# Optimization experiments

Measured on AMD Instinct MI355X. Metric: run time of the kernel, lower is better.

Reference implementation:

```python
import jax, jax.numpy as jnp
import numpy as np

DECAY = 0.99
EPSILON = 1e-05
CODEBOOK_SIZE = 1024


def setup_inputs() -> dict:
    key = jax.random.key(0)
    k1, k2, k3 = jax.random.split(key, 3)
    B, T, D, K = 8, 4096, 128, CODEBOOK_SIZE
    return {
        "x": jax.random.normal(k1, (B, T, D), dtype=jnp.float32),
        "embed": jax.random.normal(k2, (K, D), dtype=jnp.float32),
        "cluster_size": jnp.ones((K,), dtype=jnp.float32),
        "embed_avg": jax.random.normal(k3, (K, D), dtype=jnp.float32),
    }


def reference(x, embed, cluster_size, embed_avg):
    shape = x.shape
    K, D = embed.shape
    flat = x.reshape(-1, D)  # (N, D)

    dist = 2.0 * (flat @ embed.T) - jnp.sum(flat * flat, axis=1, keepdims=True) \
           - jnp.sum(embed * embed, axis=1)[None, :]  # (N, K)
    embed_ind_flat = jnp.argmax(dist, axis=-1)  # (N,) int
    embed_ind = embed_ind_flat.reshape(shape[:-1])
    quantize = embed[embed_ind]  # dequantize via gather, (B, T, D)

    # training EMA updates (one-hot scatter expressed as segment sums)
    counts = jax.ops.segment_sum(jnp.ones_like(embed_ind_flat, dtype=x.dtype),
                                 embed_ind_flat, num_segments=K)  # == onehot.sum(0)
    embed_sum = jax.ops.segment_sum(flat, embed_ind_flat, num_segments=K)  # == (x.T @ onehot).T

    new_cluster_size = cluster_size * DECAY + (1.0 - DECAY) * counts
    new_embed_avg = embed_avg * DECAY + (1.0 - DECAY) * embed_sum

    total = new_cluster_size.sum()
    smoothed = (new_cluster_size + EPSILON) / (total + K * EPSILON) * total
    new_embed = new_embed_avg / smoothed[:, None]

    return quantize, embed_ind, new_cluster_size, new_embed_avg, new_embed
```

## Files before the change

kernel.cpp:

```cpp
#include <hip/hip_runtime.h>

#define NROWS 32768
#define DDIM  128
#define KCODES 1024
#define DECAY 0.99f
#define OMD   0.01f
#define EPS   1e-5f

typedef __attribute__((ext_vector_type(8))) short short8;
typedef __attribute__((ext_vector_type(4))) float f32x4;

#define WS_COUNTS 0
#define WS_OFFS   1024
#define WS_CURSOR 2048
#define WS_INV    3072
#define WS_EN2H   4096
#define WS_BUCKET 5120

__device__ __forceinline__ unsigned int f2bf(float f) {
  union { float f; unsigned int u; } cv; cv.f = f;
  unsigned int u = cv.u;
  return (u + 0x7fffu + ((u >> 16) & 1u)) >> 16;
}

__global__ __launch_bounds__(256) void pack_e(const float* __restrict__ embed,
                                              ushort* __restrict__ epack,
                                              float* __restrict__ en2h,
                                              int* __restrict__ cnt0) {
  const int tid = threadIdx.x;
  if (blockIdx.x == 0) {
    #pragma unroll
    for (int i = 0; i < 4; ++i) cnt0[tid + i * 256] = 0;
  }
  const int w = tid >> 6, lane = tid & 63;
  const int nt = blockIdx.x * 4 + w;
  const int m = lane & 15, q = lane >> 4;
  const int row = nt * 16 + m;
  const float* ep = embed + (size_t)row * DDIM + q * 8;
  float ss = 0.f;
  #pragma unroll
  for (int kb = 0; kb < 4; ++kb) {
    float4 v0 = *(const float4*)(ep + kb * 32);
    float4 v1 = *(const float4*)(ep + kb * 32 + 4);
    float v[8] = {v0.x, v0.y, v0.z, v0.w, v1.x, v1.y, v1.z, v1.w};
    unsigned int h[8], l[8];
    #pragma unroll
    for (int j = 0; j < 8; ++j) {
      ss += v[j] * v[j];
      h[j] = f2bf(v[j]);
      float fh = __uint_as_float(h[j] << 16);
      l[j] = f2bf(v[j] - fh);
    }
    uint4 ph, pl;
    ph.x = h[0] | (h[1] << 16); ph.y = h[2] | (h[3] << 16);
    ph.z = h[4] | (h[5] << 16); ph.w = h[6] | (h[7] << 16);
    pl.x = l[0] | (l[1] << 16); pl.y = l[2] | (l[3] << 16);
    pl.z = l[4] | (l[5] << 16); pl.w = l[6] | (l[7] << 16);
    *(uint4*)(epack + (((size_t)nt * 8 + kb) * 64 + lane) * 8)     = ph;
    *(uint4*)(epack + (((size_t)nt * 8 + kb + 4) * 64 + lane) * 8) = pl;
  }
  ss += __shfl_xor(ss, 16, 64);
  ss += __shfl_xor(ss, 32, 64);
  if (q == 0) en2h[row] = 0.5f * ss;
}

__global__ __launch_bounds__(256) void vq_mfma(
    const float* __restrict__ x, const short8* __restrict__ ep8,
    const float* __restrict__ en2h, const float* __restrict__ embed,
    float* __restrict__ out_ind, float* __restrict__ out_q,
    int* __restrict__ cnt_i) {
  __shared__ unsigned long long keys[4][32];
  __shared__ int scodes[32];
  const int tid = threadIdx.x;
  const int w = tid >> 6, lane = tid & 63;
  const int c = lane & 15, q = lane >> 4;
  const int mt0 = blockIdx.x * 2;

  short8 a[2][8];
  #pragma unroll
  for (int t = 0; t < 2; ++t) {
    const float* xp = x + (size_t)((mt0 + t) * 16 + c) * DDIM + q * 8;
    #pragma unroll
    for (int kb = 0; kb < 4; ++kb) {
      float4 v0 = *(const float4*)(xp + kb * 32);
      float4 v1 = *(const float4*)(xp + kb * 32 + 4);
      float v[8] = {v0.x, v0.y, v0.z, v0.w, v1.x, v1.y, v1.z, v1.w};
      short8 hh, ll;
      #pragma unroll
      for (int j = 0; j < 8; ++j) {
        unsigned int hv = f2bf(v[j]);
        hh[j] = (short)hv;
        float fh = __uint_as_float(hv << 16);
        ll[j] = (short)f2bf(v[j] - fh);
      }
      a[t][kb] = hh;
      a[t][kb + 4] = ll;
    }
  }

  float bestv[8]; int besti[8];
  #pragma unroll
  for (int i = 0; i < 8; ++i) { bestv[i] = -3.4e38f; besti[i] = 0; }

  const int nt0 = w * 16;
  const int ph = blockIdx.x & 15;

  auto stage = [&](short8 (&st)[8], float& nh, int i) {
    const int nt = nt0 + ((ph + i) & 15);
    const short8* p = ep8 + (size_t)nt * 512 + lane;
    #pragma unroll
    for (int j = 0; j < 8; ++j) st[j] = p[j * 64];
    nh = en2h[nt * 16 + c];
  };

  auto proc = [&](const short8 (&st)[8], float nh, int i) {
    const int nt = nt0 + ((ph + i) & 15);
    f32x4 acc0 = {-nh, -nh, -nh, -nh};
    f32x4 acc1 = acc0;
    __builtin_amdgcn_s_setprio(1);
    #pragma unroll
    for (int kb = 0; kb < 4; ++kb) {
      acc0 = __builtin_amdgcn_mfma_f32_16x16x32_bf16(a[0][kb], st[kb], acc0, 0, 0, 0);
      acc1 = __builtin_amdgcn_mfma_f32_16x16x32_bf16(a[1][kb], st[kb], acc1, 0, 0, 0);
    }
    #pragma unroll
    for (int kb = 0; kb < 4; ++kb) {
      acc0 = __builtin_amdgcn_mfma_f32_16x16x32_bf16(a[0][kb + 4], st[kb], acc0, 0, 0, 0);
      acc1 = __builtin_amdgcn_mfma_f32_16x16x32_bf16(a[1][kb + 4], st[kb], acc1, 0, 0, 0);
    }
    #pragma unroll
    for (int kb = 0; kb < 4; ++kb) {
      acc0 = __builtin_amdgcn_mfma_f32_16x16x32_bf16(a[0][kb], st[kb + 4], acc0, 0, 0, 0);
      acc1 = __builtin_amdgcn_mfma_f32_16x16x32_bf16(a[1][kb], st[kb + 4], acc1, 0, 0, 0);
    }
    __builtin_amdgcn_s_setprio(0);
    const int code = nt * 16 + c;
    #pragma unroll
    for (int r = 0; r < 4; ++r) {
      float v0 = acc0[r];
      if (v0 > bestv[r] || (v0 == bestv[r] && code < besti[r])) {
        bestv[r] = v0; besti[r] = code;
      }
      float v1 = acc1[r];
      if (v1 > bestv[4 + r] || (v1 == bestv[4 + r] && code < besti[4 + r])) {
        bestv[4 + r] = v1; besti[4 + r] = code;
      }
    }
  };

  short8 sA[8], sB[8];
  float nhA, nhB;
  stage(sA, nhA, 0);

  for (int i = 0; i < 14; i += 2) {
    stage(sB, nhB, i + 1);
    __builtin_amdgcn_sched_barrier(0);
    proc(sA, nhA, i);
    stage(sA, nhA, i + 2);
    __builtin_amdgcn_sched_barrier(0);
    proc(sB, nhB, i + 1);
  }
  stage(sB, nhB, 15);
  __builtin_amdgcn_sched_barrier(0);
  proc(sA, nhA, 14);
  proc(sB, nhB, 15);

  #pragma unroll
  for (int off = 1; off < 16; off <<= 1) {
    #pragma unroll
    for (int i = 0; i < 8; ++i) {
      float ov = __shfl_xor(bestv[i], off, 64);
      int   oi = __shfl_xor(besti[i], off, 64);
      if (ov > bestv[i] || (ov == bestv[i] && oi < besti[i])) {
        bestv[i] = ov; besti[i] = oi;
      }
    }
  }
  if (c == 0) {
    #pragma unroll
    for (int t = 0; t < 2; ++t)
      #pragma unroll
      for (int r = 0; r < 4; ++r) {
        unsigned u = __float_as_uint(bestv[t * 4 + r]);
        unsigned su = (u & 0x80000000u) ? ~u : (u | 0x80000000u);
        keys[w][t * 16 + q * 4 + r] =
            ((unsigned long long)su << 32) |
            (unsigned long long)(0xFFFFFFFFu - (unsigned)besti[t * 4 + r]);
      }
  }
  __syncthreads();
  if (tid < 32) {
    unsigned long long k0 = keys[0][tid], k1 = keys[1][tid];
    unsigned long long k2 = keys[2][tid], k3 = keys[3][tid];
    unsigned long long k = k0 > k1 ? k0 : k1;
    if (k2 > k) k = k2;
    if (k3 > k) k = k3;
    int code = (int)(0xFFFFFFFFu - (unsigned)(k & 0xFFFFFFFFull));
    out_ind[blockIdx.x * 32 + tid] = (float)code;
    scodes[tid] = code;
    atomicAdd(&cnt_i[code], 1);
  }
  __syncthreads();
  #pragma unroll
  for (int it = 0; it < 4; ++it) {
    int idx = tid + it * 256;
    int row = idx >> 5, c4 = idx & 31;
    int code = scodes[row];
    *(float4*)(out_q + (size_t)(blockIdx.x * 32 + row) * DDIM + c4 * 4) =
        *(const float4*)(embed + (size_t)code * DDIM + c4 * 4);
  }
}

__global__ __launch_bounds__(1024) void scan_fin(
    int* offs, const float* __restrict__ cs,
    float* __restrict__ counts_g, int* __restrict__ cursor,
    float* __restrict__ inv, float* __restrict__ out_ncs) {
  __shared__ float wtot[16], ctot[16];
  const int tid = threadIdx.x;
  const int lane = tid & 63, w = tid >> 6;
  const int cnt = offs[tid];
  const float cnum = (float)cnt;
  const float cv = cs[tid];
  float s = cnum;
  #pragma unroll
  for (int off = 1; off < 64; off <<= 1) {
    float v = __shfl_up(s, off, 64);
    if (lane >= off) s += v;
  }
  float r2 = cv;
  #pragma unroll
  for (int off = 32; off > 0; off >>= 1) r2 += __shfl_down(r2, off, 64);
  if (lane == 63) wtot[w] = s;
  if (lane == 0)  ctot[w] = r2;
  __syncthreads();
  if (tid < 16) {
    float v = wtot[tid];
    #pragma unroll
    for (int off = 1; off < 16; off <<= 1) {
      float p = __shfl_up(v, off, 64);
      if (tid >= off) v += p;
    }
    wtot[tid] = v;
    float t2 = ctot[tid];
    #pragma unroll
    for (int off = 8; off > 0; off >>= 1) t2 += __shfl_down(t2, off, 64);
    if (tid == 0) ctot[0] = t2;
  }
  __syncthreads();
  const float prefix = (w > 0) ? wtot[w - 1] : 0.f;
  const int excl = (int)(s + prefix) - cnt;
  offs[tid] = excl;
  cursor[tid] = excl;
  counts_g[tid] = cnum;
  const float ncs = cv * DECAY + OMD * cnum;
  out_ncs[tid] = ncs;
  const float total = ctot[0] * DECAY + OMD * (float)NROWS;
  inv[tid] = (total + (float)KCODES * EPS) / ((ncs + EPS) * total);
}

__global__ void scatter_rows(const float* __restrict__ out_ind,
                             int* __restrict__ cursor, int* __restrict__ bucket) {
  int row = blockIdx.x * 256 + threadIdx.x;
  int code = (int)out_ind[row];
  int pos = atomicAdd(cursor + code, 1);
  bucket[pos] = row;
}

__global__ __launch_bounds__(256) void esum_fin(
    const int* __restrict__ bucket, const int* __restrict__ offs,
    const float* __restrict__ counts, const float* __restrict__ x,
    const float* __restrict__ ea, const float* __restrict__ inv,
    float* __restrict__ out_nea, float* __restrict__ out_ne) {
  __shared__ float4 part[512];
  const int code = blockIdx.x;
  const int t = threadIdx.x;
  const int c8 = t & 15;
  const int h = t >> 4;
  const int start = offs[code];
  const int cnt = (int)counts[code];
  float4 a0 = {0.f, 0.f, 0.f, 0.f}, a1 = {0.f, 0.f, 0.f, 0.f};
  int i = h;
  for (; i + 16 < cnt; i += 32) {
    int rowA = bucket[start + i];
    int rowB = bucket[start + i + 16];
    const float* pa = x + (size_t)rowA * DDIM + c8 * 8;
    const float* pb = x + (size_t)rowB * DDIM + c8 * 8;
    float4 xa0 = *(const float4*)(pa), xa1 = *(const float4*)(pa + 4);
    float4 xb0 = *(const float4*)(pb), xb1 = *(const float4*)(pb + 4);
    a0.x += xa0.x + xb0.x; a0.y += xa0.y + xb0.y; a0.z += xa0.z + xb0.z; a0.w += xa0.w + xb0.w;
    a1.x += xa1.x + xb1.x; a1.y += xa1.y + xb1.y; a1.z += xa1.z + xb1.z; a1.w += xa1.w + xb1.w;
  }
  for (; i < cnt; i += 16) {
    int row = bucket[start + i];
    const float* pa = x + (size_t)row * DDIM + c8 * 8;
    float4 xa0 = *(const float4*)(pa), xa1 = *(const float4*)(pa + 4);
    a0.x += xa0.x; a0.y += xa0.y; a0.z += xa0.z; a0.w += xa0.w;
    a1.x += xa1.x; a1.y += xa1.y; a1.z += xa1.z; a1.w += xa1.w;
  }
  part[h * 32 + c8 * 2]     = a0;
  part[h * 32 + c8 * 2 + 1] = a1;
  __syncthreads();
  if (t < 32) {
    float4 s = part[t];
    #pragma unroll
    for (int hh = 1; hh < 16; ++hh) {
      float4 p = part[hh * 32 + t];
      s.x += p.x; s.y += p.y; s.z += p.z; s.w += p.w;
    }
    float iv = inv[code];
    int base = code * DDIM + t * 4;
    float4 a = *(const float4*)(ea + base);
    float4 nea;
    nea.x = a.x * DECAY + OMD * s.x; nea.y = a.y * DECAY + OMD * s.y;
    nea.z = a.z * DECAY + OMD * s.z; nea.w = a.w * DECAY + OMD * s.w;
    *(float4*)(out_nea + base) = nea;
    float4 ne;
    ne.x = nea.x * iv; ne.y = nea.y * iv; ne.z = nea.z * iv; ne.w = nea.w * iv;
    *(float4*)(out_ne + base) = ne;
  }
}

extern "C" void kernel_launch(void* const* d_in, const int* in_sizes, int n_in,
                              void* d_out, int out_size, void* d_ws, size_t ws_size,
                              hipStream_t stream) {
  const float* x     = (const float*)d_in[0];
  const float* embed = (const float*)d_in[1];
  const float* cs    = (const float*)d_in[2];
  const float* ea    = (const float*)d_in[3];

  float* out     = (float*)d_out;
  float* out_q   = out;
  float* out_ind = out_q + 4194304;
  float* out_ncs = out_ind + 32768;
  float* out_nea = out_ncs + 1024;
  float* out_ne  = out_nea + 131072;

  float* ws     = (float*)d_ws;
  float* counts = ws + WS_COUNTS;
  int*   offs   = (int*)(ws + WS_OFFS);
  int*   cursor = (int*)(ws + WS_CURSOR);
  float* inv    = ws + WS_INV;
  float* en2h   = ws + WS_EN2H;
  int*   bucket = (int*)(ws + WS_BUCKET);

  ushort* epack = (ushort*)out_nea;

  pack_e<<<16, 256, 0, stream>>>(embed, epack, en2h, offs);
  vq_mfma<<<NROWS / 32, 256, 0, stream>>>(x, (const short8*)epack, en2h, embed,
                                          out_ind, out_q, offs);
  scan_fin<<<1, 1024, 0, stream>>>(offs, cs, counts, cursor, inv, out_ncs);
  scatter_rows<<<NROWS / 256, 256, 0, stream>>>(out_ind, cursor, bucket);
  esum_fin<<<KCODES, 256, 0, stream>>>(bucket, offs, counts, x, ea, inv,
                                       out_nea, out_ne);
}
```

Measured before the change: 166.1 us.

## Replace global bucket sort with per-code scan of indices in esum kernel

```diff
diff --git a/kernel.cpp b/kernel.cpp
--- a/kernel.cpp
+++ b/kernel.cpp
@@ -10,12 +10,8 @@
 typedef __attribute__((ext_vector_type(8))) short short8;
 typedef __attribute__((ext_vector_type(4))) float f32x4;
 
-#define WS_COUNTS 0
-#define WS_OFFS   1024
-#define WS_CURSOR 2048
-#define WS_INV    3072
-#define WS_EN2H   4096
-#define WS_BUCKET 5120
+#define WS_CSSUM 0
+#define WS_EN2H  1024
 
 __device__ __forceinline__ unsigned int f2bf(float f) {
   union { float f; unsigned int u; } cv; cv.f = f;
@@ -26,12 +22,10 @@
 __global__ __launch_bounds__(256) void pack_e(const float* __restrict__ embed,
                                               ushort* __restrict__ epack,
                                               float* __restrict__ en2h,
-                                              int* __restrict__ cnt0) {
+                                              const float* __restrict__ cs,
+                                              float* __restrict__ cssum) {
+  __shared__ float ws4[4];
   const int tid = threadIdx.x;
-  if (blockIdx.x == 0) {
-    #pragma unroll
-    for (int i = 0; i < 4; ++i) cnt0[tid + i * 256] = 0;
-  }
   const int w = tid >> 6, lane = tid & 63;
   const int nt = blockIdx.x * 4 + w;
   const int m = lane & 15, q = lane >> 4;
@@ -62,13 +56,21 @@
   ss += __shfl_xor(ss, 16, 64);
   ss += __shfl_xor(ss, 32, 64);
   if (q == 0) en2h[row] = 0.5f * ss;
+
+  if (blockIdx.x == 0) {
+    float s = cs[tid] + cs[tid + 256] + cs[tid + 512] + cs[tid + 768];
+    #pragma unroll
+    for (int off = 1; off < 64; off <<= 1) s += __shfl_xor(s, off, 64);
+    if (lane == 0) ws4[w] = s;
+    __syncthreads();
+    if (tid == 0) cssum[0] = ws4[0] + ws4[1] + ws4[2] + ws4[3];
+  }
 }
 
 __global__ __launch_bounds__(256) void vq_mfma(
     const float* __restrict__ x, const short8* __restrict__ ep8,
     const float* __restrict__ en2h, const float* __restrict__ embed,
-    float* __restrict__ out_ind, float* __restrict__ out_q,
-    int* __restrict__ cnt_i) {
+    float* __restrict__ out_ind, float* __restrict__ out_q) {
   __shared__ unsigned long long keys[4][32];
   __shared__ int scodes[32];
   const int tid = threadIdx.x;
@@ -103,18 +105,15 @@
   for (int i = 0; i < 8; ++i) { bestv[i] = -3.4e38f; besti[i] = 0; }
 
   const int nt0 = w * 16;
-  const int ph = blockIdx.x & 15;
 
   auto stage = [&](short8 (&st)[8], float& nh, int i) {
-    const int nt = nt0 + ((ph + i) & 15);
-    const short8* p = ep8 + (size_t)nt * 512 + lane;
+    const short8* p = ep8 + (size_t)(nt0 + i) * 512 + lane;
     #pragma unroll
     for (int j = 0; j < 8; ++j) st[j] = p[j * 64];
-    nh = en2h[nt * 16 + c];
+    nh = en2h[(nt0 + i) * 16 + c];
   };
 
   auto proc = [&](const short8 (&st)[8], float nh, int i) {
-    const int nt = nt0 + ((ph + i) & 15);
     f32x4 acc0 = {-nh, -nh, -nh, -nh};
     f32x4 acc1 = acc0;
     __builtin_amdgcn_s_setprio(1);
@@ -134,36 +133,31 @@
       acc1 = __builtin_amdgcn_mfma_f32_16x16x32_bf16(a[1][kb], st[kb + 4], acc1, 0, 0, 0);
     }
     __builtin_amdgcn_s_setprio(0);
-    const int code = nt * 16 + c;
+    const int code = (nt0 + i) * 16 + c;
     #pragma unroll
     for (int r = 0; r < 4; ++r) {
-      float v0 = acc0[r];
-      if (v0 > bestv[r] || (v0 == bestv[r] && code < besti[r])) {
-        bestv[r] = v0; besti[r] = code;
-      }
-      float v1 = acc1[r];
-      if (v1 > bestv[4 + r] || (v1 == bestv[4 + r] && code < besti[4 + r])) {
-        bestv[4 + r] = v1; besti[4 + r] = code;
-      }
+      if (acc0[r] > bestv[r])     { bestv[r] = acc0[r];     besti[r] = code; }
+      if (acc1[r] > bestv[4 + r]) { bestv[4 + r] = acc1[r]; besti[4 + r] = code; }
     }
   };
 
-  short8 sA[8], sB[8];
-  float nhA, nhB;
+  short8 sA[8], sB[8], sC[8];
+  float nhA, nhB, nhC;
   stage(sA, nhA, 0);
-
-  for (int i = 0; i < 14; i += 2) {
-    stage(sB, nhB, i + 1);
+  stage(sB, nhB, 1);
+
+  for (int t = 0; t < 15; t += 3) {
+    stage(sC, nhC, t + 2);
     __builtin_amdgcn_sched_barrier(0);
-    proc(sA, nhA, i);
-    stage(sA, nhA, i + 2);
+    proc(sA, nhA, t);
+    stage(sA, nhA, (t + 3 > 15) ? 15 : t + 3);
     __builtin_amdgcn_sched_barrier(0);
-    proc(sB, nhB, i + 1);
-  }
-  stage(sB, nhB, 15);
-  __builtin_amdgcn_sched_barrier(0);
-  proc(sA, nhA, 14);
-  proc(sB, nhB, 15);
+    proc(sB, nhB, t + 1);
+    stage(sB, nhB, (t + 4 > 15) ? 15 : t + 4);
+    __builtin_amdgcn_sched_barrier(0);
+    proc(sC, nhC, t + 2);
+  }
+  proc(sA, nhA, 15);
 
   #pragma unroll
   for (int off = 1; off < 16; off <<= 1) {
@@ -198,7 +192,6 @@
     int code = (int)(0xFFFFFFFFu - (unsigned)(k & 0xFFFFFFFFull));
     out_ind[blockIdx.x * 32 + tid] = (float)code;
     scodes[tid] = code;
-    atomicAdd(&cnt_i[code], 1);
   }
   __syncthreads();
   #pragma unroll
@@ -211,91 +204,61 @@
   }
 }
 
-__global__ __launch_bounds__(1024) void scan_fin(
-    int* offs, const float* __restrict__ cs,
-    float* __restrict__ counts_g, int* __restrict__ cursor,
-    float* __restrict__ inv, float* __restrict__ out_ncs) {
-  __shared__ float wtot[16], ctot[16];
-  const int tid = threadIdx.x;
-  const int lane = tid & 63, w = tid >> 6;
-  const int cnt = offs[tid];
-  const float cnum = (float)cnt;
-  const float cv = cs[tid];
-  float s = cnum;
-  #pragma unroll
-  for (int off = 1; off < 64; off <<= 1) {
-    float v = __shfl_up(s, off, 64);
-    if (lane >= off) s += v;
-  }
-  float r2 = cv;
-  #pragma unroll
-  for (int off = 32; off > 0; off >>= 1) r2 += __shfl_down(r2, off, 64);
-  if (lane == 63) wtot[w] = s;
-  if (lane == 0)  ctot[w] = r2;
-  __syncthreads();
-  if (tid < 16) {
-    float v = wtot[tid];
-    #pragma unroll
-    for (int off = 1; off < 16; off <<= 1) {
-      float p = __shfl_up(v, off, 64);
-      if (tid >= off) v += p;
-    }
-    wtot[tid] = v;
-    float t2 = ctot[tid];
-    #pragma unroll
-    for (int off = 8; off > 0; off >>= 1) t2 += __shfl_down(t2, off, 64);
-    if (tid == 0) ctot[0] = t2;
-  }
-  __syncthreads();
-  const float prefix = (w > 0) ? wtot[w - 1] : 0.f;
-  const int excl = (int)(s + prefix) - cnt;
-  offs[tid] = excl;
-  cursor[tid] = excl;
-  counts_g[tid] = cnum;
-  const float ncs = cv * DECAY + OMD * cnum;
-  out_ncs[tid] = ncs;
-  const float total = ctot[0] * DECAY + OMD * (float)NROWS;
-  inv[tid] = (total + (float)KCODES * EPS) / ((ncs + EPS) * total);
-}
-
-__global__ void scatter_rows(const float* __restrict__ out_ind,
-                             int* __restrict__ cursor, int* __restrict__ bucket) {
-  int row = blockIdx.x * 256 + threadIdx.x;
-  int code = (int)out_ind[row];
-  int pos = atomicAdd(cursor + code, 1);
-  bucket[pos] = row;
-}
-
+#define LCAP 4096
 __global__ __launch_bounds__(256) void esum_fin(
-    const int* __restrict__ bucket, const int* __restrict__ offs,
-    const float* __restrict__ counts, const float* __restrict__ x,
-    const float* __restrict__ ea, const float* __restrict__ inv,
-    float* __restrict__ out_nea, float* __restrict__ out_ne) {
+    const float* __restrict__ out_ind, const float* __restrict__ x,
+    const float* __restrict__ cs, const float* __restrict__ ea,
+    const float* __restrict__ cssum,
+    float* __restrict__ out_ncs, float* __restrict__ out_nea,
+    float* __restrict__ out_ne) {
+  __shared__ int list[LCAP];
+  __shared__ int lcnt;
   __shared__ float4 part[512];
   const int code = blockIdx.x;
   const int t = threadIdx.x;
   const int c8 = t & 15;
   const int h = t >> 4;
-  const int start = offs[code];
-  const int cnt = (int)counts[code];
+  if (t == 0) lcnt = 0;
+  __syncthreads();
+  #pragma unroll 4
+  for (int i = 0; i < 128; ++i) {
+    int row = i * 256 + t;
+    if ((int)out_ind[row] == code) {
+      int p = atomicAdd(&lcnt, 1);
+      if (p < LCAP) list[p] = row;
+    }
+  }
+  __syncthreads();
+  const int cnt = lcnt;
   float4 a0 = {0.f, 0.f, 0.f, 0.f}, a1 = {0.f, 0.f, 0.f, 0.f};
-  int i = h;
-  for (; i + 16 < cnt; i += 32) {
-    int rowA = bucket[start + i];
-    int rowB = bucket[start + i + 16];
-    const float* pa = x + (size_t)rowA * DDIM + c8 * 8;
-    const float* pb = x + (size_t)rowB * DDIM + c8 * 8;
-    float4 xa0 = *(const float4*)(pa), xa1 = *(const float4*)(pa + 4);
-    float4 xb0 = *(const float4*)(pb), xb1 = *(const float4*)(pb + 4);
-    a0.x += xa0.x + xb0.x; a0.y += xa0.y + xb0.y; a0.z += xa0.z + xb0.z; a0.w += xa0.w + xb0.w;
-    a1.x += xa1.x + xb1.x; a1.y += xa1.y + xb1.y; a1.z += xa1.z + xb1.z; a1.w += xa1.w + xb1.w;
-  }
-  for (; i < cnt; i += 16) {
-    int row = bucket[start + i];
-    const float* pa = x + (size_t)row * DDIM + c8 * 8;
-    float4 xa0 = *(const float4*)(pa), xa1 = *(const float4*)(pa + 4);
-    a0.x += xa0.x; a0.y += xa0.y; a0.z += xa0.z; a0.w += xa0.w;
-    a1.x += xa1.x; a1.y += xa1.y; a1.z += xa1.z; a1.w += xa1.w;
+  if (cnt <= LCAP) {
+    int i = h;
+    for (; i + 16 < cnt; i += 32) {
+      int rowA = list[i];
+      int rowB = list[i + 16];
+      const float* pa = x + (size_t)rowA * DDIM + c8 * 8;
+      const float* pb = x + (size_t)rowB * DDIM + c8 * 8;
+      float4 xa0 = *(const float4*)(pa), xa1 = *(const float4*)(pa + 4);
+      float4 xb0 = *(const float4*)(pb), xb1 = *(const float4*)(pb + 4);
+      a0.x += xa0.x + xb0.x; a0.y += xa0.y + xb0.y; a0.z += xa0.z + xb0.z; a0.w += xa0.w + xb0.w;
+      a1.x += xa1.x + xb1.x; a1.y += xa1.y + xb1.y; a1.z += xa1.z + xb1.z; a1.w += xa1.w + xb1.w;
+    }
+    for (; i < cnt; i += 16) {
+      int row = list[i];
+      const float* pa = x + (size_t)row * DDIM + c8 * 8;
+      float4 xa0 = *(const float4*)(pa), xa1 = *(const float4*)(pa + 4);
+      a0.x += xa0.x; a0.y += xa0.y; a0.z += xa0.z; a0.w += xa0.w;
+      a1.x += xa1.x; a1.y += xa1.y; a1.z += xa1.z; a1.w += xa1.w;
+    }
+  } else {
+    for (int row = h; row < NROWS; row += 16) {
+      if ((int)out_ind[row] == code) {
+        const float* pa = x + (size_t)row * DDIM + c8 * 8;
+        float4 xa0 = *(const float4*)(pa), xa1 = *(const float4*)(pa + 4);
+        a0.x += xa0.x; a0.y += xa0.y; a0.z += xa0.z; a0.w += xa0.w;
+        a1.x += xa1.x; a1.y += xa1.y; a1.z += xa1.z; a1.w += xa1.w;
+      }
+    }
   }
   part[h * 32 + c8 * 2]     = a0;
   part[h * 32 + c8 * 2 + 1] = a1;
@@ -307,7 +270,10 @@
       float4 p = part[hh * 32 + t];
       s.x += p.x; s.y += p.y; s.z += p.z; s.w += p.w;
     }
-    float iv = inv[code];
+    const float ncs = cs[code] * DECAY + OMD * (float)cnt;
+    const float total = cssum[0] * DECAY + OMD * (float)NROWS;
+    const float iv = (total + (float)KCODES * EPS) / ((ncs + EPS) * total);
+    if (t == 0) out_ncs[code] = ncs;
     int base = code * DDIM + t * 4;
     float4 a = *(const float4*)(ea + base);
     float4 nea;
@@ -336,20 +302,14 @@
   float* out_ne  = out_nea + 131072;
 
   float* ws     = (float*)d_ws;
-  float* counts = ws + WS_COUNTS;
-  int*   offs   = (int*)(ws + WS_OFFS);
-  int*   cursor = (int*)(ws + WS_CURSOR);
-  float* inv    = ws + WS_INV;
+  float* cssum  = ws + WS_CSSUM;
   float* en2h   = ws + WS_EN2H;
-  int*   bucket = (int*)(ws + WS_BUCKET);
 
   ushort* epack = (ushort*)out_nea;
 
-  pack_e<<<16, 256, 0, stream>>>(embed, epack, en2h, offs);
+  pack_e<<<16, 256, 0, stream>>>(embed, epack, en2h, cs, cssum);
   vq_mfma<<<NROWS / 32, 256, 0, stream>>>(x, (const short8*)epack, en2h, embed,
-                                          out_ind, out_q, offs);
-  scan_fin<<<1, 1024, 0, stream>>>(offs, cs, counts, cursor, inv, out_ncs);
-  scatter_rows<<<NROWS / 256, 256, 0, stream>>>(out_ind, cursor, bucket);
-  esum_fin<<<KCODES, 256, 0, stream>>>(bucket, offs, counts, x, ea, inv,
-                                       out_nea, out_ne);
-}
+                                          out_ind, out_q);
+  esum_fin<<<KCODES, 256, 0, stream>>>(out_ind, x, cs, ea, cssum,
+                                       out_ncs, out_nea, out_ne);
+}
```

Result: slower. 172.9 us (+4.1%).
